# Performance work log

Hardware: AMD Instinct MI355X
Metric: run time of the kernel (lower is better)

Reference implementation:

```python
import jax, jax.numpy as jnp
import numpy as np
import math

D_MODEL = 1024
N_HEADS = 16
DH = D_MODEL // N_HEADS
THETA = 10000.0


def _rope_tables(S):
    # freqs: (dh/2,)
    inv_freq = 1.0 / (THETA ** (jnp.arange(0, DH, 2, dtype=jnp.float32) / DH))
    ang = jnp.arange(S, dtype=jnp.float32)[:, None] * inv_freq[None, :]  # (S, dh/2)
    cos = jnp.concatenate([jnp.cos(ang), jnp.cos(ang)], axis=-1)  # (S, dh)
    sin = jnp.concatenate([jnp.sin(ang), jnp.sin(ang)], axis=-1)
    return cos, sin


def _apply_rope(x, cos, sin):
    # x: (B, S, H, dh); rotate-half RoPE
    x1, x2 = jnp.split(x, 2, axis=-1)
    rot = jnp.concatenate([-x2, x1], axis=-1)
    c = cos[None, :, None, :]
    s = sin[None, :, None, :]
    return x * c + rot * s


def setup_inputs() -> dict:
    key = jax.random.key(0)
    k1, k2, k3 = jax.random.split(key, 3)
    x = jax.random.normal(k1, (4, 2048, D_MODEL), dtype=jnp.float32)
    qkv = 0.01 * jax.random.normal(k2, (3 * D_MODEL, D_MODEL), dtype=jnp.float32)
    wo = 0.01 * jax.random.normal(k3, (D_MODEL, D_MODEL), dtype=jnp.float32)
    return {"x": x, "qkv": qkv, "wo": wo}


def reference(x, qkv, wo):
    B, S, D = x.shape
    QKV = x @ qkv.T  # (B, S, 3D)
    Q, K, V = jnp.split(QKV, 3, axis=-1)
    q = Q.reshape(B, S, N_HEADS, DH)
    k = K.reshape(B, S, N_HEADS, DH)
    v = V.reshape(B, S, N_HEADS, DH)
    cos, sin = _rope_tables(S)
    q = _apply_rope(q, cos, sin)
    k = _apply_rope(k, cos, sin)
    # (B, H, S, dh)
    q = q.transpose(0, 2, 1, 3)
    k = k.transpose(0, 2, 1, 3)
    v = v.transpose(0, 2, 1, 3)
    scores = jnp.einsum("bhsd,bhtd->bhst", q, k) / math.sqrt(float(DH))
    mask = jnp.tril(jnp.ones((S, S), dtype=scores.dtype))
    scores = scores * mask
    # faithful to original: any exact-zero entry (masked or incidental) -> -inf
    scores = jnp.where(scores == 0.0, -jnp.inf, scores)
    attn = jax.nn.softmax(scores, axis=-1)
    out = jnp.einsum("bhst,bhtd->bhsd", attn, v)  # (B, H, S, dh)
    out = out.transpose(0, 2, 1, 3).reshape(B, S, D)
    return out @ wo.T
```

## Files before the change

kernel.cpp:

```cpp
#include <hip/hip_runtime.h>
#include <math.h>

typedef __bf16 bf16x8 __attribute__((ext_vector_type(8)));
typedef __bf16 bf16x4 __attribute__((ext_vector_type(4)));
typedef float  floatx4 __attribute__((ext_vector_type(4)));
typedef float  floatx2 __attribute__((ext_vector_type(2)));

#define AS1(p) ((__attribute__((address_space(1))) void*)(p))
#define AS3(p) ((__attribute__((address_space(3))) void*)(p))

#define MASKV (-1.0e30f)
#define SOFTMAX_SCALE_LOG2 0.1803368801111244f
#define ROPE_LOG2F 0.4152410118609203f

__global__ __launch_bounds__(256)
void cvt3_kernel(const float* __restrict__ x, const float* __restrict__ qkv,
                 const float* __restrict__ wo, __bf16* __restrict__ xb,
                 __bf16* __restrict__ qkvb, __bf16* __restrict__ wob,
                 float* __restrict__ rt)
{
    const int bi = blockIdx.x;
    if (bi >= 12288) {
        const int e0 = (bi - 12288) * 1024 + threadIdx.x * 4;
#pragma unroll
        for (int j = 0; j < 4; ++j) {
            const int e = e0 + j;
            const int s = e >> 5, d = e & 31;
            const float f = exp2f(-(float)d * ROPE_LOG2F);
            float sn, cs;
            sincosf((float)s * f, &sn, &cs);
            floatx2 t; t[0] = cs; t[1] = sn;
            *(floatx2*)(rt + e * 2) = t;
        }
        return;
    }
    const float* src;
    __bf16* dst;
    int base;
    if (bi < 8192)       { src = x;   dst = xb;   base = bi * 1024; }
    else if (bi < 11264) { src = qkv; dst = qkvb; base = (bi - 8192) * 1024; }
    else                 { src = wo;  dst = wob;  base = (bi - 11264) * 1024; }

    const int i = base + threadIdx.x * 4;
    const floatx4 v = *(const floatx4*)(src + i);
    bf16x4 o;
    o[0] = (__bf16)v[0]; o[1] = (__bf16)v[1];
    o[2] = (__bf16)v[2]; o[3] = (__bf16)v[3];
    *(bf16x4*)(dst + i) = o;
}

__global__ __launch_bounds__(256)
void gemm_rope_kernel(const __bf16* __restrict__ A, const __bf16* __restrict__ BT,
                      __bf16* __restrict__ Qr, __bf16* __restrict__ Kr,
                      __bf16* __restrict__ Vt, const float* __restrict__ rt)
{
    const int K = 1024;
    __shared__ __align__(16) __bf16 As[128 * 32];
    __shared__ __align__(16) __bf16 Bs[128 * 32];

    const int tid  = threadIdx.x;
    const int wave = tid >> 6;
    const int lane = tid & 63;
    const int quad = lane >> 4;
    const int l16  = lane & 15;

    const long m0 = (long)blockIdx.y * 128;
    const long n0 = (long)blockIdx.x * 128;
    const int  wm = (wave >> 1) * 64;
    const int  wn = (wave & 1) * 64;

    floatx4 acc[4][4] = {};

    for (int k0 = 0; k0 < K; k0 += 32) {
#pragma unroll
        for (int t = 0; t < 2; ++t) {
            const int c   = (t * 4 + wave) * 64 + lane;
            const int row = c >> 2;
            const int kc  = (c & 3) * 8;
            const __bf16* ga = A  + (m0 + row) * (long)K + k0 + kc;
            const __bf16* gb = BT + (n0 + row) * (long)K + k0 + kc;
            __builtin_amdgcn_global_load_lds(AS1(ga), AS3(As + (t * 4 + wave) * 512), 16, 0, 0);
            __builtin_amdgcn_global_load_lds(AS1(gb), AS3(Bs + (t * 4 + wave) * 512), 16, 0, 0);
        }
        asm volatile("s_waitcnt vmcnt(0)" ::: "memory");
        __syncthreads();

        bf16x8 af[4], bfq[4];
#pragma unroll
        for (int mt = 0; mt < 4; ++mt)
            af[mt] = *(const bf16x8*)(As + (wm + mt * 16 + l16) * 32 + quad * 8);
#pragma unroll
        for (int nt = 0; nt < 4; ++nt)
            bfq[nt] = *(const bf16x8*)(Bs + (wn + nt * 16 + l16) * 32 + quad * 8);

#pragma unroll
        for (int mt = 0; mt < 4; ++mt)
#pragma unroll
            for (int nt = 0; nt < 4; ++nt)
                acc[mt][nt] = __builtin_amdgcn_mfma_f32_16x16x32_bf16(
                    af[mt], bfq[nt], acc[mt][nt], 0, 0, 0);
        __syncthreads();
    }

    const int gn0    = (int)n0 + wn;
    const int region = gn0 >> 10;
    const int h      = (gn0 >> 6) & 15;

    if (region == 2) {
#pragma unroll
        for (int mt = 0; mt < 4; ++mt) {
            const long gm = m0 + wm + mt * 16 + quad * 4;
            const int  b  = (int)(gm >> 11), s = (int)(gm & 2047);
#pragma unroll
            for (int nt = 0; nt < 4; ++nt) {
                const int d = nt * 16 + l16;
                bf16x4 w;
#pragma unroll
                for (int r = 0; r < 4; ++r) w[r] = (__bf16)acc[mt][nt][r];
                *(bf16x4*)(Vt + ((size_t)(b * 16 + h) * 64 + d) * 2048 + s) = w;
            }
        }
    } else {
        __bf16* dst = region ? Kr : Qr;
#pragma unroll
        for (int nt = 0; nt < 2; ++nt) {
            const int d1 = nt * 16 + l16;
#pragma unroll
            for (int mt = 0; mt < 4; ++mt) {
                const long gm0 = m0 + wm + mt * 16 + quad * 4;
                const int  b   = (int)(gm0 >> 11), s0 = (int)(gm0 & 2047);
#pragma unroll
                for (int r = 0; r < 4; ++r) {
                    const floatx2 t = *(const floatx2*)(rt + ((s0 + r) * 32 + d1) * 2);
                    const float a1 = acc[mt][nt][r];
                    const float a2 = acc[mt][nt + 2][r];
                    __bf16* row = dst + ((size_t)((b * 16 + h) * 2048 + s0 + r)) * 64;
                    row[d1]      = (__bf16)(a1 * t[0] - a2 * t[1]);
                    row[d1 + 32] = (__bf16)(a2 * t[0] + a1 * t[1]);
                }
            }
        }
    }
}

__global__ __launch_bounds__(256)
void gemm_bt_kernel(const __bf16* __restrict__ A, const __bf16* __restrict__ BT,
                    float* __restrict__ C, int M, int N, int K)
{
    __shared__ __align__(16) __bf16 As[128 * 32];
    __shared__ __align__(16) __bf16 Bs[128 * 32];

    const int tid  = threadIdx.x;
    const int wave = tid >> 6;
    const int lane = tid & 63;
    const int quad = lane >> 4;
    const int l16  = lane & 15;

    const long m0 = (long)blockIdx.y * 128;
    const long n0 = (long)blockIdx.x * 128;
    const int  wm = (wave >> 1) * 64;
    const int  wn = (wave & 1) * 64;

    floatx4 acc[4][4] = {};

    for (int k0 = 0; k0 < K; k0 += 32) {
#pragma unroll
        for (int t = 0; t < 2; ++t) {
            const int c   = (t * 4 + wave) * 64 + lane;
            const int row = c >> 2;
            const int kc  = (c & 3) * 8;
            const __bf16* ga = A  + (m0 + row) * (long)K + k0 + kc;
            const __bf16* gb = BT + (n0 + row) * (long)K + k0 + kc;
            __builtin_amdgcn_global_load_lds(AS1(ga), AS3(As + (t * 4 + wave) * 512), 16, 0, 0);
            __builtin_amdgcn_global_load_lds(AS1(gb), AS3(Bs + (t * 4 + wave) * 512), 16, 0, 0);
        }
        asm volatile("s_waitcnt vmcnt(0)" ::: "memory");
        __syncthreads();

        bf16x8 af[4], bfq[4];
#pragma unroll
        for (int mt = 0; mt < 4; ++mt)
            af[mt] = *(const bf16x8*)(As + (wm + mt * 16 + l16) * 32 + quad * 8);
#pragma unroll
        for (int nt = 0; nt < 4; ++nt)
            bfq[nt] = *(const bf16x8*)(Bs + (wn + nt * 16 + l16) * 32 + quad * 8);

#pragma unroll
        for (int mt = 0; mt < 4; ++mt)
#pragma unroll
            for (int nt = 0; nt < 4; ++nt)
                acc[mt][nt] = __builtin_amdgcn_mfma_f32_16x16x32_bf16(
                    af[mt], bfq[nt], acc[mt][nt], 0, 0, 0);
        __syncthreads();
    }

#pragma unroll
    for (int mt = 0; mt < 4; ++mt)
#pragma unroll
        for (int nt = 0; nt < 4; ++nt) {
            const long row = m0 + wm + mt * 16 + quad * 4;
            const long col = n0 + wn + nt * 16 + l16;
#pragma unroll
            for (int r = 0; r < 4; ++r)
                C[(row + r) * (long)N + col] = acc[mt][nt][r];
        }
}

__global__ __launch_bounds__(256, 4)
void attn_kernel(const __bf16* __restrict__ Qr, const __bf16* __restrict__ Kr,
                 const __bf16* __restrict__ Vt, __bf16* __restrict__ ctx)
{
    __shared__ __align__(16) __bf16 Ks[64 * 64];
    __shared__ __align__(16) __bf16 Vs[64 * 64];
    __shared__ __align__(16) __bf16 plds[4][16 * 72];

    const int bh   = blockIdx.x;
    const int b    = bh >> 4, h = bh & 15;
    const int tid  = threadIdx.x;
    const int wave = tid >> 6;
    const int lane = tid & 63;
    const int quad = lane >> 4, l16 = lane & 15;
    const int sw   = l16 & 7;

    const __bf16* Qb = Qr + (size_t)bh * 2048 * 64;
    const __bf16* Kb = Kr + (size_t)bh * 2048 * 64;
    const __bf16* Vb = Vt + (size_t)bh * 64 * 2048;
    __bf16* Pw = &plds[wave][0];

    const int c0   = tid;
    const int row0 = c0 >> 3, jg0 = (c0 & 7) ^ (row0 & 7);
    const int c1   = 256 + tid;
    const int row1 = c1 >> 3, jg1 = (c1 & 7) ^ (row1 & 7);

    const int tiles[2] = { (int)blockIdx.y, 31 - (int)blockIdx.y };

    for (int pass = 0; pass < 2; ++pass) {
        const int q0b  = tiles[pass] * 64;
        const int q0   = q0b + wave * 16;
        const int qa   = q0 + l16;
        const int kend = q0b + 64;

        bf16x8 bq[2];
#pragma unroll
        for (int t = 0; t < 2; ++t)
            bq[t] = *(const bf16x8*)(Qb + (q0 + l16) * 64 + t * 32 + quad * 8);

        floatx4 o[4] = {};
        float lpart = 0.f;

        for (int kt = 0; kt < kend; kt += 64) {
            __builtin_amdgcn_global_load_lds(AS1(Kb + (size_t)(kt + row0) * 64 + jg0 * 8),
                                             AS3(Ks + wave * 512), 16, 0, 0);
            __builtin_amdgcn_global_load_lds(AS1(Vb + (size_t)row0 * 2048 + kt + jg0 * 8),
                                             AS3(Vs + wave * 512), 16, 0, 0);
            __builtin_amdgcn_global_load_lds(AS1(Kb + (size_t)(kt + row1) * 64 + jg1 * 8),
                                             AS3(Ks + (4 + wave) * 512), 16, 0, 0);
            __builtin_amdgcn_global_load_lds(AS1(Vb + (size_t)row1 * 2048 + kt + jg1 * 8),
                                             AS3(Vs + (4 + wave) * 512), 16, 0, 0);
            asm volatile("s_waitcnt vmcnt(0)" ::: "memory");
            __syncthreads();

            floatx4 s[4] = {};
#pragma unroll
            for (int st = 0; st < 4; ++st) {
                bf16x8 ka0 = *(const bf16x8*)(Ks + (st * 16 + l16) * 64 + ((0 + quad) ^ sw) * 8);
                bf16x8 ka1 = *(const bf16x8*)(Ks + (st * 16 + l16) * 64 + ((4 + quad) ^ sw) * 8);
                s[st] = __builtin_amdgcn_mfma_f32_16x16x32_bf16(ka0, bq[0], s[st], 0, 0, 0);
                s[st] = __builtin_amdgcn_mfma_f32_16x16x32_bf16(ka1, bq[1], s[st], 0, 0, 0);
            }

#pragma unroll
            for (int st = 0; st < 4; ++st) {
                bf16x4 w;
#pragma unroll
                for (int r = 0; r < 4; ++r) {
                    const int key = kt + st * 16 + quad * 4 + r;
                    const float v = (key > qa) ? MASKV : s[st][r] * SOFTMAX_SCALE_LOG2;
                    const float p = __builtin_amdgcn_exp2f(v);
                    lpart += p;
                    w[r] = (__bf16)p;
                }
                *(bf16x4*)(Pw + l16 * 72 + st * 16 + quad * 4) = w;
            }

            asm volatile("s_waitcnt lgkmcnt(0)" ::: "memory");
            bf16x8 ap0 = *(const bf16x8*)(Pw + l16 * 72 + quad * 8);
            bf16x8 ap1 = *(const bf16x8*)(Pw + l16 * 72 + 32 + quad * 8);

#pragma unroll
            for (int nt = 0; nt < 4; ++nt) {
                bf16x8 bv0 = *(const bf16x8*)(Vs + (nt * 16 + l16) * 64 + ((0 + quad) ^ sw) * 8);
                bf16x8 bv1 = *(const bf16x8*)(Vs + (nt * 16 + l16) * 64 + ((4 + quad) ^ sw) * 8);
                o[nt] = __builtin_amdgcn_mfma_f32_16x16x32_bf16(ap0, bv0, o[nt], 0, 0, 0);
                o[nt] = __builtin_amdgcn_mfma_f32_16x16x32_bf16(ap1, bv1, o[nt], 0, 0, 0);
            }

            __syncthreads();
        }

        float l = lpart;
        l += __shfl_xor(l, 16, 64);
        l += __shfl_xor(l, 32, 64);
        float lr[4];
#pragma unroll
        for (int r = 0; r < 4; ++r)
            lr[r] = __shfl(l, quad * 4 + r, 64);
#pragma unroll
        for (int nt = 0; nt < 4; ++nt)
#pragma unroll
            for (int r = 0; r < 4; ++r) {
                const int srow = q0 + quad * 4 + r;
                const float inv_l = 1.0f / fmaxf(lr[r], 1e-20f);
                ctx[((size_t)(b * 2048 + srow)) * 1024 + h * 64 + nt * 16 + l16] =
                    (__bf16)(o[nt][r] * inv_l);
            }
    }
}

extern "C" void kernel_launch(void* const* d_in, const int* in_sizes, int n_in,
                              void* d_out, int out_size, void* d_ws, size_t ws_size,
                              hipStream_t stream)
{
    const float* x   = (const float*)d_in[0];
    const float* qkv = (const float*)d_in[1];
    const float* wo  = (const float*)d_in[2];
    float* out = (float*)d_out;

    char* ws = (char*)d_ws;
    const size_t MB = 1024 * 1024;
    __bf16* xb   = (__bf16*)(ws);
    __bf16* qkvb = (__bf16*)(ws + 16 * MB);
    __bf16* wob  = (__bf16*)(ws + 22 * MB);
    __bf16* Qr   = (__bf16*)(ws + 24 * MB);
    __bf16* Kr   = (__bf16*)(ws + 40 * MB);
    __bf16* Vt   = (__bf16*)(ws + 56 * MB);
    __bf16* ctx  = (__bf16*)(ws + 72 * MB);
    float*  rt   = (float*) (ws + 88 * MB);

    cvt3_kernel<<<12352, 256, 0, stream>>>(x, qkv, wo, xb, qkvb, wob, rt);
    gemm_rope_kernel<<<dim3(24, 64), 256, 0, stream>>>(xb, qkvb, Qr, Kr, Vt, rt);
    attn_kernel<<<dim3(64, 16), 256, 0, stream>>>(Qr, Kr, Vt, ctx);
    gemm_bt_kernel<<<dim3(8, 64), 256, 0, stream>>>(ctx, wob, out, 8192, 1024, 1024);
}
```

Before: 258.8 us.

## Rewrite both GEMMs with double-buffered, swizzled 128x256 pipelined tiles

Both projection GEMMs now share one device routine that uses 512-thread blocks with 128x256 output tiles and a K-step of 64. LDS is double-buffered and XOR-swizzled, and global-to-LDS loads for the next tiles are interleaved with MFMA phases behind explicit barriers and raised wave priority. Blocks are remapped so that neighbouring M tiles land on the same XCD to improve L2 reuse. The aim is to hide global-load latency and cut LDS bank conflicts and per-iteration syncs, at the cost of 96 KB of dynamic LDS per block (occupancy limited to 2 blocks) and a fragile hand-written wait schedule.

```diff
diff --git a/kernel.cpp b/kernel.cpp
--- a/kernel.cpp
+++ b/kernel.cpp
@@ -12,6 +12,10 @@
 #define MASKV (-1.0e30f)
 #define SOFTMAX_SCALE_LOG2 0.1803368801111244f
 #define ROPE_LOG2F 0.4152410118609203f
+
+#define BARRIER do { __builtin_amdgcn_sched_barrier(0); \
+                     __builtin_amdgcn_s_barrier(); \
+                     __builtin_amdgcn_sched_barrier(0); } while (0)
 
 __global__ __launch_bounds__(256)
 void cvt3_kernel(const float* __restrict__ x, const float* __restrict__ qkv,
@@ -49,91 +53,164 @@
     *(bf16x4*)(dst + i) = o;
 }
 
-__global__ __launch_bounds__(256)
-void gemm_rope_kernel(const __bf16* __restrict__ A, const __bf16* __restrict__ BT,
-                      __bf16* __restrict__ Qr, __bf16* __restrict__ Kr,
-                      __bf16* __restrict__ Vt, const float* __restrict__ rt)
-{
-    const int K = 1024;
-    __shared__ __align__(16) __bf16 As[128 * 32];
-    __shared__ __align__(16) __bf16 Bs[128 * 32];
-
+__device__ __forceinline__ void gemm_pipe(const __bf16* __restrict__ Ap,
+                                          const __bf16* __restrict__ Bp,
+                                          const int m0, const int n0,
+                                          __bf16* smem, floatx4 (&acc)[4][4])
+{
     const int tid  = threadIdx.x;
     const int wave = tid >> 6;
     const int lane = tid & 63;
     const int quad = lane >> 4;
     const int l16  = lane & 15;
-
-    const long m0 = (long)blockIdx.y * 128;
-    const long n0 = (long)blockIdx.x * 128;
-    const int  wm = (wave >> 1) * 64;
-    const int  wn = (wave & 1) * 64;
+    const int wr   = wave >> 2;
+    const int wc   = wave & 3;
+
+    const int arow = wr * 32 + l16;
+    const int brow = (wc & 1) * 64 + l16;
+    const int bsel = (wc >> 1) * 8192;
+    const int swz  = (l16 & 7) << 4;
+    int coff[2];
+    coff[0] = (( (quad << 4))        ^ swz) >> 1;
+    coff[1] = ((64 | (quad << 4))    ^ swz) >> 1;
+
+    auto stageA = [&](int buf, int h, int k0) {
+        const int o = tid << 4;
+        const int r = o >> 7;
+        const int c = (o & 127) ^ ((r & 7) << 4);
+        const __bf16* src = Ap + (size_t)(m0 + h * 64 + r) * 1024 + k0 + (c >> 1);
+        __builtin_amdgcn_global_load_lds(AS1(src),
+            AS3(smem + buf * 24576 + h * 4096 + wave * 512), 16, 0, 0);
+    };
+    auto stageB = [&](int buf, int h, int k0) {
+#pragma unroll
+        for (int q = 0; q < 2; ++q) {
+            const int o = (q * 512 + tid) << 4;
+            const int r = o >> 7;
+            const int c = (o & 127) ^ ((r & 7) << 4);
+            const __bf16* src = Bp + (size_t)(n0 + h * 128 + r) * 1024 + k0 + (c >> 1);
+            __builtin_amdgcn_global_load_lds(AS1(src),
+                AS3(smem + buf * 24576 + 8192 + h * 8192 + (q * 8 + wave) * 512), 16, 0, 0);
+        }
+    };
+
+#define RDA(P, qm, fm, ks) (*(const bf16x8*)(smem + (P) * 24576 + (qm) * 4096 \
+                             + ((arow + (fm) * 16) << 6) + coff[ks]))
+#define RDB(P, g, ks)      (*(const bf16x8*)(smem + (P) * 24576 + 8192 + bsel \
+                             + ((brow + (g) * 16) << 6) + coff[ks]))
+#define MFMA8(MB, NB, AV, BV) do { \
+    _Pragma("unroll") for (int fm_ = 0; fm_ < 2; ++fm_) \
+    _Pragma("unroll") for (int gi_ = 0; gi_ < 2; ++gi_) \
+    _Pragma("unroll") for (int ks_ = 0; ks_ < 2; ++ks_) \
+        acc[(MB) + fm_][(NB) + gi_] = __builtin_amdgcn_mfma_f32_16x16x32_bf16( \
+            AV[fm_][ks_], BV[gi_][ks_], acc[(MB) + fm_][(NB) + gi_], 0, 0, 0); \
+} while (0)
+
+    stageA(0, 0, 0);  stageB(0, 0, 0);  stageA(0, 1, 0);  stageB(0, 1, 0);
+    stageA(1, 0, 64); stageB(1, 0, 64); stageA(1, 1, 64);
+    asm volatile("s_waitcnt vmcnt(4)" ::: "memory");
+    BARRIER;
+
+    bf16x8 a0[2][2], a1[2][2], b0[2][2], b1[2][2];
+
+#define TILE(JT, P) do { \
+    const int kn_ = ((JT) + 2) * 64; \
+     \
+    _Pragma("unroll") for (int f_ = 0; f_ < 2; ++f_) \
+    _Pragma("unroll") for (int k_ = 0; k_ < 2; ++k_) a0[f_][k_] = RDA(P, 0, f_, k_); \
+    _Pragma("unroll") for (int g_ = 0; g_ < 2; ++g_) \
+    _Pragma("unroll") for (int k_ = 0; k_ < 2; ++k_) b0[g_][k_] = RDB(P, g_, k_); \
+    if ((JT) + 1 < 16) stageB(1 - (P), 1, ((JT) + 1) * 64); \
+    BARRIER; \
+    __builtin_amdgcn_s_setprio(1); MFMA8(0, 0, a0, b0); __builtin_amdgcn_s_setprio(0); \
+    BARRIER; \
+     \
+    _Pragma("unroll") for (int g_ = 0; g_ < 2; ++g_) \
+    _Pragma("unroll") for (int k_ = 0; k_ < 2; ++k_) b1[g_][k_] = RDB(P, 2 + g_, k_); \
+    if ((JT) + 2 < 16) stageA(P, 0, kn_); \
+    BARRIER; \
+    __builtin_amdgcn_s_setprio(1); MFMA8(0, 2, a0, b1); __builtin_amdgcn_s_setprio(0); \
+    BARRIER; \
+     \
+    _Pragma("unroll") for (int f_ = 0; f_ < 2; ++f_) \
+    _Pragma("unroll") for (int k_ = 0; k_ < 2; ++k_) a1[f_][k_] = RDA(P, 1, f_, k_); \
+    if ((JT) + 2 < 16) stageB(P, 0, kn_); \
+    BARRIER; \
+    __builtin_amdgcn_s_setprio(1); MFMA8(2, 2, a1, b1); __builtin_amdgcn_s_setprio(0); \
+    BARRIER; \
+     \
+    if ((JT) + 2 < 16) stageA(P, 1, kn_); \
+    BARRIER; \
+    __builtin_amdgcn_s_setprio(1); MFMA8(2, 0, a1, b0); __builtin_amdgcn_s_setprio(0); \
+     \
+    if ((JT) + 2 < 16)      { asm volatile("s_waitcnt vmcnt(4)" ::: "memory"); } \
+    else if ((JT) + 1 < 16) { asm volatile("s_waitcnt vmcnt(0)" ::: "memory"); } \
+    BARRIER; \
+} while (0)
+
+    for (int it = 0; it < 8; ++it) {
+        TILE(2 * it, 0);
+        TILE(2 * it + 1, 1);
+    }
+#undef TILE
+#undef RDA
+#undef RDB
+#undef MFMA8
+}
+
+__global__ __launch_bounds__(512, 2)
+void gemm_rope_kernel(const __bf16* __restrict__ A, const __bf16* __restrict__ BT,
+                      __bf16* __restrict__ Qr, __bf16* __restrict__ Kr,
+                      __bf16* __restrict__ Vt, const float* __restrict__ rt)
+{
+    extern __shared__ __align__(16) __bf16 smem[];
+    const int id  = blockIdx.x;
+    const int xcd = id & 7, lid = id >> 3;
+    const int tm  = xcd * 8 + lid / 12;
+    const int tn  = lid % 12;
+    const int m0  = tm * 128, n0 = tn * 256;
 
     floatx4 acc[4][4] = {};
-
-    for (int k0 = 0; k0 < K; k0 += 32) {
-#pragma unroll
-        for (int t = 0; t < 2; ++t) {
-            const int c   = (t * 4 + wave) * 64 + lane;
-            const int row = c >> 2;
-            const int kc  = (c & 3) * 8;
-            const __bf16* ga = A  + (m0 + row) * (long)K + k0 + kc;
-            const __bf16* gb = BT + (n0 + row) * (long)K + k0 + kc;
-            __builtin_amdgcn_global_load_lds(AS1(ga), AS3(As + (t * 4 + wave) * 512), 16, 0, 0);
-            __builtin_amdgcn_global_load_lds(AS1(gb), AS3(Bs + (t * 4 + wave) * 512), 16, 0, 0);
-        }
-        asm volatile("s_waitcnt vmcnt(0)" ::: "memory");
-        __syncthreads();
-
-        bf16x8 af[4], bfq[4];
-#pragma unroll
-        for (int mt = 0; mt < 4; ++mt)
-            af[mt] = *(const bf16x8*)(As + (wm + mt * 16 + l16) * 32 + quad * 8);
-#pragma unroll
-        for (int nt = 0; nt < 4; ++nt)
-            bfq[nt] = *(const bf16x8*)(Bs + (wn + nt * 16 + l16) * 32 + quad * 8);
-
-#pragma unroll
-        for (int mt = 0; mt < 4; ++mt)
-#pragma unroll
-            for (int nt = 0; nt < 4; ++nt)
-                acc[mt][nt] = __builtin_amdgcn_mfma_f32_16x16x32_bf16(
-                    af[mt], bfq[nt], acc[mt][nt], 0, 0, 0);
-        __syncthreads();
-    }
-
-    const int gn0    = (int)n0 + wn;
+    gemm_pipe(A, BT, m0, n0, smem, acc);
+
+    const int tid  = threadIdx.x;
+    const int wave = tid >> 6;
+    const int lane = tid & 63;
+    const int quad = lane >> 4, l16 = lane & 15;
+    const int wr   = wave >> 2, wc = wave & 3;
+
+    const int gn0    = n0 + wc * 64;
     const int region = gn0 >> 10;
     const int h      = (gn0 >> 6) & 15;
 
     if (region == 2) {
 #pragma unroll
-        for (int mt = 0; mt < 4; ++mt) {
-            const long gm = m0 + wm + mt * 16 + quad * 4;
-            const int  b  = (int)(gm >> 11), s = (int)(gm & 2047);
-#pragma unroll
-            for (int nt = 0; nt < 4; ++nt) {
-                const int d = nt * 16 + l16;
+        for (int f = 0; f < 4; ++f) {
+            const int gm = m0 + (f >> 1) * 64 + wr * 32 + (f & 1) * 16 + quad * 4;
+            const int b = gm >> 11, s = gm & 2047;
+#pragma unroll
+            for (int g = 0; g < 4; ++g) {
+                const int d = g * 16 + l16;
                 bf16x4 w;
 #pragma unroll
-                for (int r = 0; r < 4; ++r) w[r] = (__bf16)acc[mt][nt][r];
+                for (int r = 0; r < 4; ++r) w[r] = (__bf16)acc[f][g][r];
                 *(bf16x4*)(Vt + ((size_t)(b * 16 + h) * 64 + d) * 2048 + s) = w;
             }
         }
     } else {
         __bf16* dst = region ? Kr : Qr;
 #pragma unroll
-        for (int nt = 0; nt < 2; ++nt) {
-            const int d1 = nt * 16 + l16;
-#pragma unroll
-            for (int mt = 0; mt < 4; ++mt) {
-                const long gm0 = m0 + wm + mt * 16 + quad * 4;
-                const int  b   = (int)(gm0 >> 11), s0 = (int)(gm0 & 2047);
+        for (int g = 0; g < 2; ++g) {
+            const int d1 = g * 16 + l16;
+#pragma unroll
+            for (int f = 0; f < 4; ++f) {
+                const int gm0 = m0 + (f >> 1) * 64 + wr * 32 + (f & 1) * 16 + quad * 4;
+                const int b = gm0 >> 11, s0 = gm0 & 2047;
 #pragma unroll
                 for (int r = 0; r < 4; ++r) {
                     const floatx2 t = *(const floatx2*)(rt + ((s0 + r) * 32 + d1) * 2);
-                    const float a1 = acc[mt][nt][r];
-                    const float a2 = acc[mt][nt + 2][r];
+                    const float a1 = acc[f][g][r];
+                    const float a2 = acc[f][g + 2][r];
                     __bf16* row = dst + ((size_t)((b * 16 + h) * 2048 + s0 + r)) * 64;
                     row[d1]      = (__bf16)(a1 * t[0] - a2 * t[1]);
                     row[d1 + 32] = (__bf16)(a2 * t[0] + a1 * t[1]);
@@ -143,67 +220,36 @@
     }
 }
 
-__global__ __launch_bounds__(256)
+__global__ __launch_bounds__(512, 2)
 void gemm_bt_kernel(const __bf16* __restrict__ A, const __bf16* __restrict__ BT,
-                    float* __restrict__ C, int M, int N, int K)
-{
-    __shared__ __align__(16) __bf16 As[128 * 32];
-    __shared__ __align__(16) __bf16 Bs[128 * 32];
+                    float* __restrict__ C)
+{
+    extern __shared__ __align__(16) __bf16 smem[];
+    const int id  = blockIdx.x;
+    const int xcd = id & 7, lid = id >> 3;
+    const int tm  = xcd * 8 + (lid >> 2);
+    const int tn  = lid & 3;
+    const int m0  = tm * 128, n0 = tn * 256;
+
+    floatx4 acc[4][4] = {};
+    gemm_pipe(A, BT, m0, n0, smem, acc);
 
     const int tid  = threadIdx.x;
-    const int wave = tid >> 6;
-    const int lane = tid & 63;
-    const int quad = lane >> 4;
-    const int l16  = lane & 15;
-
-    const long m0 = (long)blockIdx.y * 128;
-    const long n0 = (long)blockIdx.x * 128;
-    const int  wm = (wave >> 1) * 64;
-    const int  wn = (wave & 1) * 64;
-
-    floatx4 acc[4][4] = {};
-
-    for (int k0 = 0; k0 < K; k0 += 32) {
-#pragma unroll
-        for (int t = 0; t < 2; ++t) {
-            const int c   = (t * 4 + wave) * 64 + lane;
-            const int row = c >> 2;
-            const int kc  = (c & 3) * 8;
-            const __bf16* ga = A  + (m0 + row) * (long)K + k0 + kc;
-            const __bf16* gb = BT + (n0 + row) * (long)K + k0 + kc;
-            __builtin_amdgcn_global_load_lds(AS1(ga), AS3(As + (t * 4 + wave) * 512), 16, 0, 0);
-            __builtin_amdgcn_global_load_lds(AS1(gb), AS3(Bs + (t * 4 + wave) * 512), 16, 0, 0);
-        }
-        asm volatile("s_waitcnt vmcnt(0)" ::: "memory");
-        __syncthreads();
-
-        bf16x8 af[4], bfq[4];
-#pragma unroll
-        for (int mt = 0; mt < 4; ++mt)
-            af[mt] = *(const bf16x8*)(As + (wm + mt * 16 + l16) * 32 + quad * 8);
-#pragma unroll
-        for (int nt = 0; nt < 4; ++nt)
-            bfq[nt] = *(const bf16x8*)(Bs + (wn + nt * 16 + l16) * 32 + quad * 8);
-
-#pragma unroll
-        for (int mt = 0; mt < 4; ++mt)
-#pragma unroll
-            for (int nt = 0; nt < 4; ++nt)
-                acc[mt][nt] = __builtin_amdgcn_mfma_f32_16x16x32_bf16(
-                    af[mt], bfq[nt], acc[mt][nt], 0, 0, 0);
-        __syncthreads();
-    }
-
-#pragma unroll
-    for (int mt = 0; mt < 4; ++mt)
-#pragma unroll
-        for (int nt = 0; nt < 4; ++nt) {
-            const long row = m0 + wm + mt * 16 + quad * 4;
-            const long col = n0 + wn + nt * 16 + l16;
+    const int wave = tid >> 6, lane = tid & 63;
+    const int quad = lane >> 4, l16 = lane & 15;
+    const int wr   = wave >> 2, wc = wave & 3;
+
+#pragma unroll
+    for (int f = 0; f < 4; ++f) {
+        const int row = m0 + (f >> 1) * 64 + wr * 32 + (f & 1) * 16 + quad * 4;
+#pragma unroll
+        for (int g = 0; g < 4; ++g) {
+            const int col = n0 + wc * 64 + g * 16 + l16;
 #pragma unroll
             for (int r = 0; r < 4; ++r)
-                C[(row + r) * (long)N + col] = acc[mt][nt][r];
-        }
+                C[(size_t)(row + r) * 1024 + col] = acc[f][g][r];
+        }
+    }
 }
 
 __global__ __launch_bounds__(256, 4)
@@ -337,8 +383,13 @@
     __bf16* ctx  = (__bf16*)(ws + 72 * MB);
     float*  rt   = (float*) (ws + 88 * MB);
 
+    hipFuncSetAttribute((const void*)gemm_rope_kernel,
+                        hipFuncAttributeMaxDynamicSharedMemorySize, 98304);
+    hipFuncSetAttribute((const void*)gemm_bt_kernel,
+                        hipFuncAttributeMaxDynamicSharedMemorySize, 98304);
+
     cvt3_kernel<<<12352, 256, 0, stream>>>(x, qkv, wo, xb, qkvb, wob, rt);
-    gemm_rope_kernel<<<dim3(24, 64), 256, 0, stream>>>(xb, qkvb, Qr, Kr, Vt, rt);
+    gemm_rope_kernel<<<768, 512, 98304, stream>>>(xb, qkvb, Qr, Kr, Vt, rt);
     attn_kernel<<<dim3(64, 16), 256, 0, stream>>>(Qr, Kr, Vt, ctx);
-    gemm_bt_kernel<<<dim3(8, 64), 256, 0, stream>>>(ctx, wob, out, 8192, 1024, 1024);
-}
+    gemm_bt_kernel<<<256, 512, 98304, stream>>>(ctx, wob, out);
+}
```

Result: faster. 229.8 us (-11.2%).
